# Optimization experiments

Measured on AMD Instinct MI355X. Metric: run time of the kernel, lower is better.

The kernel has to match this reference:

```python
import jax, jax.numpy as jnp
import numpy as np

B, S, H, DH = 1, 4096, 8, 40  # hardcoded in the original forward
D = H * DH  # 320

def setup_inputs() -> dict:
    key = jax.random.key(0)
    ks = jax.random.split(key, 6)
    s = 1.0 / np.sqrt(D)
    return {
        "x": jax.random.normal(ks[0], (B, S, D), dtype=jnp.float32),
        "Wq": jax.random.normal(ks[1], (D, D), dtype=jnp.float32) * s,
        "Wk": jax.random.normal(ks[2], (D, D), dtype=jnp.float32) * s,
        "Wv": jax.random.normal(ks[3], (D, D), dtype=jnp.float32) * s,
        "Wo": jax.random.normal(ks[4], (D, D), dtype=jnp.float32) * s,
        "bo": jnp.zeros((D,), dtype=jnp.float32),
    }

def reference(x, Wq, Wk, Wv, Wo, bo):
    scale = DH ** (-0.5)
    # nn.Linear(bias=False): y = x @ W^T. context = x (self-attention).
    q = x @ Wq.T
    k = x @ Wk.T
    v = x @ Wv.T
    # split heads: [B,S,D] -> [B*H, S, DH]
    def split_heads(t):
        return t.reshape(B, S, H, DH).transpose(0, 2, 1, 3).reshape(B * H, S, DH)
    q, k, v = split_heads(q), split_heads(k), split_heads(v)
    # fp32 QK^T (original forces float), softmax, AV
    sim = jnp.einsum('bid,bjd->bij', q.astype(jnp.float32), k.astype(jnp.float32)) * scale
    attn = jax.nn.softmax(sim, axis=-1)
    out = jnp.einsum('bij,bjd->bid', attn, v)
    # merge heads: [B*H, S, DH] -> [B, S, D]
    out = out.reshape(B, H, S, DH).transpose(0, 2, 1, 3).reshape(B, S, D)
    return out @ Wo.T + bo
```

## Files before the change

kernel.cpp:

```cpp
#include <hip/hip_runtime.h>
#include <math.h>


#define NS 4096
#define ND 320
#define SCALE2 0.2281101152f
#define HS48 196608
#define VTH 163840
#define XN 1310720

typedef __attribute__((ext_vector_type(8))) short bf16x8;
typedef __attribute__((ext_vector_type(16))) float f32x16;

static __device__ __forceinline__ unsigned short f2bru(float f) {
  return (unsigned short)((__builtin_bit_cast(unsigned int, f) + 0x8000u) >> 16);
}
static __device__ __forceinline__ unsigned int pk2ru(float a, float b) {
  unsigned int ua = __builtin_bit_cast(unsigned int, a) + 0x8000u;
  unsigned int ub = __builtin_bit_cast(unsigned int, b) + 0x8000u;
  return __builtin_amdgcn_perm(ub, ua, 0x07060302u);
}
static __device__ __forceinline__ unsigned int pk2t(float a, float b) {
  return __builtin_amdgcn_perm(__builtin_bit_cast(unsigned int, b),
                               __builtin_bit_cast(unsigned int, a), 0x07060302u);
}
static __device__ __forceinline__ float fexp2(float x) {
  return __builtin_amdgcn_exp2f(x);
}
static __device__ __forceinline__ bf16x8 ld8(const unsigned short* p) {
  union { uint2 u[2]; bf16x8 v; } c;
  c.u[0] = *(const uint2*)p;
  c.u[1] = *(const uint2*)(p + 4);
  return c.v;
}
static __device__ __forceinline__ uint4 ld16u(const unsigned short* p) {
  uint2 a = *(const uint2*)p, b = *(const uint2*)(p + 4);
  return make_uint4(a.x, a.y, b.x, b.y);
}
static __device__ __forceinline__ void st16(unsigned short* p, uint4 v) {
  *(uint2*)p = make_uint2(v.x, v.y);
  *(uint2*)(p + 4) = make_uint2(v.z, v.w);
}
static __device__ __forceinline__ int sig32(int q) {
  int s = q >> 4, h2 = (q >> 3) & 1, j = q & 7;
  return (s << 4) | ((j >> 2) << 3) | (h2 << 2) | (j & 3);
}

__global__ __launch_bounds__(256) void proj_qkv_kernel(
    const float* __restrict__ x, const float* __restrict__ Wq,
    const float* __restrict__ Wk, const float* __restrict__ Wv,
    unsigned short* __restrict__ Qp, unsigned short* __restrict__ Kp,
    unsigned short* __restrict__ Vt) {
  const int zi = blockIdx.y;
  const int z = zi / 5;
  const int bnn = (zi - z * 5) * 64;
  const float* W = (z == 0) ? Wq : (z == 1) ? Wk : Wv;
  __shared__ __align__(16) unsigned short As[128 * 76];
  __shared__ __align__(16) unsigned short Bs[64 * 76];
  const int t = threadIdx.x;
  const int w = t >> 6, l = t & 63, l31 = l & 31, hi = l >> 5;
  const int bm = blockIdx.x * 128;
  const int m0 = w * 32;
  f32x16 acc0 = {0,0,0,0,0,0,0,0,0,0,0,0,0,0,0,0};
  f32x16 acc1 = {0,0,0,0,0,0,0,0,0,0,0,0,0,0,0,0};
  const unsigned short* af = As + (m0 + l31) * 76 + hi * 8;
  const unsigned short* bf0 = Bs + l31 * 76 + hi * 8;
  const unsigned short* bf1 = Bs + (32 + l31) * 76 + hi * 8;
  for (int k0 = 0; k0 < ND; k0 += 64) {
    __syncthreads();
#pragma unroll
    for (int i = 0; i < 4; i++) {
      int c = t + i * 256;
      int row = c >> 3, kc = (c & 7) << 3;
      const float* g = x + (bm + row) * ND + k0 + kc;
      float4 v0 = *(const float4*)g, v1 = *(const float4*)(g + 4);
      st16(As + row * 76 + kc,
           make_uint4(pk2ru(v0.x, v0.y), pk2ru(v0.z, v0.w),
                      pk2ru(v1.x, v1.y), pk2ru(v1.z, v1.w)));
    }
#pragma unroll
    for (int i = 0; i < 2; i++) {
      int c = t + i * 256;
      int row = c >> 3, kc = (c & 7) << 3;
      const float* g = W + (bnn + row) * ND + k0 + kc;
      float4 v0 = *(const float4*)g, v1 = *(const float4*)(g + 4);
      st16(Bs + row * 76 + kc,
           make_uint4(pk2ru(v0.x, v0.y), pk2ru(v0.z, v0.w),
                      pk2ru(v1.x, v1.y), pk2ru(v1.z, v1.w)));
    }
    __syncthreads();
#pragma unroll
    for (int ks = 0; ks < 4; ks++) {
      bf16x8 A = ld8(af + ks * 16);
      acc0 = __builtin_amdgcn_mfma_f32_32x32x16_bf16(A, ld8(bf0 + ks * 16), acc0, 0, 0, 0);
      acc1 = __builtin_amdgcn_mfma_f32_32x32x16_bf16(A, ld8(bf1 + ks * 16), acc1, 0, 0, 0);
    }
  }
  __syncthreads();
  if (z < 2) {
    unsigned short* Tile = As;
    unsigned short* Y = (z == 0) ? Qp : Kp;
    const float sc = (z == 0) ? SCALE2 : 1.0f;
    const unsigned int padw = (z == 0) ? 0xC200u : 0x3F80u;
#pragma unroll
    for (int r2 = 0; r2 < 16; r2++) {
      int lr = m0 + (r2 & 3) + 8 * (r2 >> 2) + 4 * hi;
      Tile[lr * 68 + l31] = f2bru(acc0[r2] * sc);
      Tile[lr * 68 + 32 + l31] = f2bru(acc1[r2] * sc);
    }
    __syncthreads();
#pragma unroll
    for (int i = 0; i < 4; i++) {
      int c = t + i * 256;
      int row = c >> 3, ch = c & 7;
      int j = bnn + ch * 8;
      int h = j / 40, dh = j - h * 40;
      uint4 v = ld16u(Tile + row * 68 + ch * 8);
      st16(Y + h * HS48 + (bm + row) * 48 + dh, v);
      if (dh == 0)
        st16(Y + h * HS48 + (bm + row) * 48 + 40, make_uint4(padw, 0u, 0u, 0u));
    }
  } else {
    unsigned short* Tile = As;
#pragma unroll
    for (int r2 = 0; r2 < 16; r2++) {
      int lr = m0 + (r2 & 3) + 8 * (r2 >> 2) + 4 * hi;
      Tile[l31 * 132 + lr] = f2bru(acc0[r2]);
      Tile[(32 + l31) * 132 + lr] = f2bru(acc1[r2]);
    }
    __syncthreads();
#pragma unroll
    for (int i = 0; i < 4; i++) {
      int c = t + i * 256;
      int row = c >> 4, ch = c & 15;
      int j = bnn + row;
      int h = j / 40, dd = j - h * 40;
      uint4 v = ld16u(Tile + row * 132 + ch * 8);
      st16(Vt + h * VTH + dd * NS + bm + ch * 8, v);
    }
  }
}

__global__ __launch_bounds__(256) void attn_kernel(
    const unsigned short* __restrict__ Qp, const unsigned short* __restrict__ Kp,
    const unsigned short* __restrict__ Vt, unsigned short* __restrict__ Op,
    float* __restrict__ Lp) {
  const int b = blockIdx.x;
  const int h = b & 7, ks = (b >> 3) & 7, qt = b >> 6;
  const int t = threadIdx.x;
  const int w = t >> 6, l = t & 63, l31 = l & 31, hi = l >> 5;
  __shared__ __align__(16) unsigned short Ks[64 * 68];
  __shared__ __align__(16) unsigned short Vs[48 * 68];
  for (int i = t; i < 272; i += 256)
    ((unsigned int*)(Vs + 40 * 68))[i] = (i < 34) ? 0x3F803F80u : 0u;

  const int kbase = ks * 512;
  const int qbase = qt * 128 + w * 32;
  const unsigned short* qp = Qp + h * HS48 + (qbase + l31) * 48 + hi * 8;
  bf16x8 qf0 = *(const bf16x8*)qp;
  bf16x8 qf1 = *(const bf16x8*)(qp + 16);
  bf16x8 qf2 = *(const bf16x8*)(qp + 32);

  f32x16 oa0 = {0,0,0,0,0,0,0,0,0,0,0,0,0,0,0,0};
  f32x16 oa1 = {0,0,0,0,0,0,0,0,0,0,0,0,0,0,0,0};

  const int kr0 = t / 6, kc0 = t - kr0 * 6;
  const int kr1 = (t + 256) / 6, kc1 = (t + 256) - kr1 * 6;
  const unsigned short* gK0 = Kp + h * HS48 + (kbase + kr0) * 48 + kc0 * 8;
  const unsigned short* gK1 = Kp + h * HS48 + (kbase + kr1) * 48 + kc1 * 8;
  unsigned short* lK0 = Ks + ((kr0 & 32) | sig32(kr0 & 31)) * 68 + kc0 * 8;
  unsigned short* lK1 = Ks + ((kr1 & 32) | sig32(kr1 & 31)) * 68 + kc1 * 8;
  const int vr0 = t >> 3, vc = t & 7, vr1 = 32 + vr0;
  const unsigned short* gV0 = Vt + h * VTH + vr0 * NS + kbase + vc * 8;
  const unsigned short* gV1 = Vt + h * VTH + vr1 * NS + kbase + vc * 8;
  unsigned short* lV0 = Vs + vr0 * 68 + vc * 8;
  unsigned short* lV1 = Vs + vr1 * 68 + vc * 8;

  const unsigned short* kf0 = Ks + l31 * 68 + hi * 8;
  const unsigned short* kf1 = Ks + (32 + l31) * 68 + hi * 8;
  const unsigned short* vf0 = Vs + l31 * 68 + hi * 8;
  const unsigned short* vf1 = Vs + (32 + (l31 & 15)) * 68 + hi * 8;

  uint4 ka = *(const uint4*)gK0;
  uint4 kb2, vb2;
  uint4 va = *(const uint4*)gV0;
  if (t < 128) kb2 = *(const uint4*)gK1;
  if (t < 64)  vb2 = *(const uint4*)gV1;

  for (int it = 0; it < 8; ++it) {
    __syncthreads();
    st16(lK0, ka);
    if (t < 128) st16(lK1, kb2);
    st16(lV0, va);
    if (t < 64) st16(lV1, vb2);
    __syncthreads();
    gK0 += 64 * 48; gK1 += 64 * 48; gV0 += 64; gV1 += 64;
    ka = *(const uint4*)gK0;
    va = *(const uint4*)gV0;
    if (t < 128) kb2 = *(const uint4*)gK1;
    if (t < 64)  vb2 = *(const uint4*)gV1;

    {
      f32x16 s0 = {0,0,0,0,0,0,0,0,0,0,0,0,0,0,0,0};
      s0 = __builtin_amdgcn_mfma_f32_32x32x16_bf16(ld8(kf0), qf0, s0, 0, 0, 0);
      s0 = __builtin_amdgcn_mfma_f32_32x32x16_bf16(ld8(kf0 + 16), qf1, s0, 0, 0, 0);
      s0 = __builtin_amdgcn_mfma_f32_32x32x16_bf16(ld8(kf0 + 32), qf2, s0, 0, 0, 0);
      unsigned int pw[8];
#pragma unroll
      for (int i = 0; i < 8; i++)
        pw[i] = pk2t(fexp2(s0[2 * i]), fexp2(s0[2 * i + 1]));
      bf16x8 pf0 = __builtin_bit_cast(bf16x8, make_uint4(pw[0], pw[1], pw[2], pw[3]));
      bf16x8 pf1 = __builtin_bit_cast(bf16x8, make_uint4(pw[4], pw[5], pw[6], pw[7]));
      oa0 = __builtin_amdgcn_mfma_f32_32x32x16_bf16(pf0, ld8(vf0), oa0, 0, 0, 0);
      oa1 = __builtin_amdgcn_mfma_f32_32x32x16_bf16(pf0, ld8(vf1), oa1, 0, 0, 0);
      oa0 = __builtin_amdgcn_mfma_f32_32x32x16_bf16(pf1, ld8(vf0 + 16), oa0, 0, 0, 0);
      oa1 = __builtin_amdgcn_mfma_f32_32x32x16_bf16(pf1, ld8(vf1 + 16), oa1, 0, 0, 0);
    }
    {
      f32x16 s1 = {0,0,0,0,0,0,0,0,0,0,0,0,0,0,0,0};
      s1 = __builtin_amdgcn_mfma_f32_32x32x16_bf16(ld8(kf1), qf0, s1, 0, 0, 0);
      s1 = __builtin_amdgcn_mfma_f32_32x32x16_bf16(ld8(kf1 + 16), qf1, s1, 0, 0, 0);
      s1 = __builtin_amdgcn_mfma_f32_32x32x16_bf16(ld8(kf1 + 32), qf2, s1, 0, 0, 0);
      unsigned int pw[8];
#pragma unroll
      for (int i = 0; i < 8; i++)
        pw[i] = pk2t(fexp2(s1[2 * i]), fexp2(s1[2 * i + 1]));
      bf16x8 pf2 = __builtin_bit_cast(bf16x8, make_uint4(pw[0], pw[1], pw[2], pw[3]));
      bf16x8 pf3 = __builtin_bit_cast(bf16x8, make_uint4(pw[4], pw[5], pw[6], pw[7]));
      oa0 = __builtin_amdgcn_mfma_f32_32x32x16_bf16(pf2, ld8(vf0 + 32), oa0, 0, 0, 0);
      oa1 = __builtin_amdgcn_mfma_f32_32x32x16_bf16(pf2, ld8(vf1 + 32), oa1, 0, 0, 0);
      oa0 = __builtin_amdgcn_mfma_f32_32x32x16_bf16(pf3, ld8(vf0 + 48), oa0, 0, 0, 0);
      oa1 = __builtin_amdgcn_mfma_f32_32x32x16_bf16(pf3, ld8(vf1 + 48), oa1, 0, 0, 0);
    }
  }

  unsigned short* opb = Op + ks * XN + h * 163840;
  float* lpb = Lp + ks * 32768 + h * NS;
#pragma unroll
  for (int r2 = 0; r2 < 16; r2++) {
    int qr = qbase + (r2 & 3) + 8 * (r2 >> 2) + 4 * hi;
    opb[qr * 40 + l31] = f2bru(oa0[r2]);
    if (l31 < 8) opb[qr * 40 + 32 + l31] = f2bru(oa1[r2]);
    if (l31 == 8) lpb[qr] = oa1[r2];
  }
}

__global__ __launch_bounds__(256) void combine_kernel(
    const unsigned short* __restrict__ Op, const float* __restrict__ Lp,
    unsigned short* __restrict__ Xo) {
  int e = (blockIdx.x * 256 + threadIdx.x) * 2;
  int h = e / 163840;
  int r = e - h * 163840;
  int s = r / 40;
  int dh = r - s * 40;
  float a0 = 0.f, a1 = 0.f, lsum = 0.f;
#pragma unroll
  for (int k = 0; k < 8; k++) {
    unsigned int u = *(const unsigned int*)(Op + k * XN + e);
    a0 += __builtin_bit_cast(float, u << 16);
    a1 += __builtin_bit_cast(float, u & 0xFFFF0000u);
    lsum += Lp[k * 32768 + h * NS + s];
  }
  float inv = 1.0f / lsum;
  *(unsigned int*)(Xo + s * ND + h * 40 + dh) = pk2ru(a0 * inv, a1 * inv);
}

__global__ __launch_bounds__(256) void proj_out_kernel(
    const unsigned short* __restrict__ Xo, const float* __restrict__ Wo,
    const float* __restrict__ bo, float* __restrict__ out) {
  __shared__ __align__(16) unsigned short As[128 * 76];
  __shared__ __align__(16) unsigned short Bs[64 * 76];
  const int t = threadIdx.x;
  const int w = t >> 6, l = t & 63, l31 = l & 31, hi = l >> 5;
  const int bm = blockIdx.x * 128;
  const int bnn = blockIdx.y * 64;
  const int m0 = w * 32;
  f32x16 acc0 = {0,0,0,0,0,0,0,0,0,0,0,0,0,0,0,0};
  f32x16 acc1 = {0,0,0,0,0,0,0,0,0,0,0,0,0,0,0,0};
  const unsigned short* af = As + (m0 + l31) * 76 + hi * 8;
  const unsigned short* bf0 = Bs + l31 * 76 + hi * 8;
  const unsigned short* bf1 = Bs + (32 + l31) * 76 + hi * 8;
  for (int k0 = 0; k0 < ND; k0 += 64) {
    __syncthreads();
#pragma unroll
    for (int i = 0; i < 4; i++) {
      int c = t + i * 256;
      int row = c >> 3, kc = (c & 7) << 3;
      uint4 v = *(const uint4*)(Xo + (bm + row) * ND + k0 + kc);
      st16(As + row * 76 + kc, v);
    }
#pragma unroll
    for (int i = 0; i < 2; i++) {
      int c = t + i * 256;
      int row = c >> 3, kc = (c & 7) << 3;
      const float* g = Wo + (bnn + row) * ND + k0 + kc;
      float4 v0 = *(const float4*)g, v1 = *(const float4*)(g + 4);
      st16(Bs + row * 76 + kc,
           make_uint4(pk2ru(v0.x, v0.y), pk2ru(v0.z, v0.w),
                      pk2ru(v1.x, v1.y), pk2ru(v1.z, v1.w)));
    }
    __syncthreads();
#pragma unroll
    for (int ks = 0; ks < 4; ks++) {
      bf16x8 A = ld8(af + ks * 16);
      acc0 = __builtin_amdgcn_mfma_f32_32x32x16_bf16(A, ld8(bf0 + ks * 16), acc0, 0, 0, 0);
      acc1 = __builtin_amdgcn_mfma_f32_32x32x16_bf16(A, ld8(bf1 + ks * 16), acc1, 0, 0, 0);
    }
  }
  const int j0 = bnn + l31, j1 = bnn + 32 + l31;
  const float bj0 = bo[j0], bj1 = bo[j1];
#pragma unroll
  for (int r2 = 0; r2 < 16; r2++) {
    int row = bm + m0 + (r2 & 3) + 8 * (r2 >> 2) + 4 * hi;
    out[row * ND + j0] = acc0[r2] + bj0;
    out[row * ND + j1] = acc1[r2] + bj1;
  }
}

extern "C" void kernel_launch(void* const* d_in, const int* in_sizes, int n_in,
                              void* d_out, int out_size, void* d_ws, size_t ws_size,
                              hipStream_t stream) {
  (void)in_sizes; (void)n_in; (void)out_size; (void)ws_size;
  const float* x  = (const float*)d_in[0];
  const float* Wq = (const float*)d_in[1];
  const float* Wk = (const float*)d_in[2];
  const float* Wv = (const float*)d_in[3];
  const float* Wo = (const float*)d_in[4];
  const float* bo = (const float*)d_in[5];
  float* out = (float*)d_out;

  unsigned short* Qp = (unsigned short*)d_ws;
  unsigned short* Kp = Qp + 8 * HS48;
  unsigned short* Vt = Kp + 8 * HS48;
  unsigned short* Xo = Vt + 8 * VTH;
  unsigned short* Op = Xo + XN;
  float* Lp = (float*)(Op + 8 * XN);

  proj_qkv_kernel<<<dim3(32, 15), 256, 0, stream>>>(x, Wq, Wk, Wv, Qp, Kp, Vt);
  attn_kernel<<<dim3(2048), 256, 0, stream>>>(Qp, Kp, Vt, Op, Lp);
  combine_kernel<<<dim3(2560), 256, 0, stream>>>(Op, Lp, Xo);
  proj_out_kernel<<<dim3(32, 5), 256, 0, stream>>>(Xo, Wo, bo, out);
}
```

Measured before the change: 131.3 us.

## Double-buffer K/V tiles in LDS and halve attention key splits

The attention kernel now uses a single LDS buffer split into two halves. The next K/V tile is written to one half while the current half feeds the MFMAs, which cuts the two barriers per iteration down to one. The key dimension is split into 4 chunks of 1024 instead of 8 of 512, halving the number of blocks and the partial outputs the combine kernel has to sum. Fewer blocks means less parallelism and longer per-block loops, and the larger LDS footprint may limit occupancy.

```diff
diff --git a/kernel.cpp b/kernel.cpp
--- a/kernel.cpp
+++ b/kernel.cpp
@@ -141,68 +141,88 @@
   }
 }
 
-__global__ __launch_bounds__(256) void attn_kernel(
+__global__ __launch_bounds__(256, 4) void attn_kernel(
     const unsigned short* __restrict__ Qp, const unsigned short* __restrict__ Kp,
     const unsigned short* __restrict__ Vt, unsigned short* __restrict__ Op,
     float* __restrict__ Lp) {
   const int b = blockIdx.x;
-  const int h = b & 7, ks = (b >> 3) & 7, qt = b >> 6;
+  const int h = b & 7, ks = (b >> 3) & 3, qt = b >> 5;
   const int t = threadIdx.x;
   const int w = t >> 6, l = t & 63, l31 = l & 31, hi = l >> 5;
-  __shared__ __align__(16) unsigned short Ks[64 * 68];
-  __shared__ __align__(16) unsigned short Vs[48 * 68];
-  for (int i = t; i < 272; i += 256)
-    ((unsigned int*)(Vs + 40 * 68))[i] = (i < 34) ? 0x3F803F80u : 0u;
-
-  const int kbase = ks * 512;
+  __shared__ __align__(16) unsigned short Lds[16384];
+  for (int i = t; i < 544; i += 256) {
+    int bsel = (i >= 272) ? 1 : 0;
+    int ui = i - bsel * 272;
+    ((unsigned int*)(Lds + bsel * 8192 + 4352 + 40 * 68))[ui] =
+        (ui < 34) ? 0x3F803F80u : 0u;
+  }
+
+  const int kbase = ks * 1024;
   const int qbase = qt * 128 + w * 32;
   const unsigned short* qp = Qp + h * HS48 + (qbase + l31) * 48 + hi * 8;
   bf16x8 qf0 = *(const bf16x8*)qp;
   bf16x8 qf1 = *(const bf16x8*)(qp + 16);
   bf16x8 qf2 = *(const bf16x8*)(qp + 32);
 
-  f32x16 oa0 = {0,0,0,0,0,0,0,0,0,0,0,0,0,0,0,0};
-  f32x16 oa1 = {0,0,0,0,0,0,0,0,0,0,0,0,0,0,0,0};
-
+  const f32x16 Z = {0,0,0,0,0,0,0,0,0,0,0,0,0,0,0,0};
+  f32x16 oa0 = Z, oa1 = Z;
+
+  const int id1 = t + 256;
+  const bool has2 = (t < 192);
   const int kr0 = t / 6, kc0 = t - kr0 * 6;
-  const int kr1 = (t + 256) / 6, kc1 = (t + 256) - kr1 * 6;
-  const unsigned short* gK0 = Kp + h * HS48 + (kbase + kr0) * 48 + kc0 * 8;
-  const unsigned short* gK1 = Kp + h * HS48 + (kbase + kr1) * 48 + kc1 * 8;
-  unsigned short* lK0 = Ks + ((kr0 & 32) | sig32(kr0 & 31)) * 68 + kc0 * 8;
-  unsigned short* lK1 = Ks + ((kr1 & 32) | sig32(kr1 & 31)) * 68 + kc1 * 8;
-  const int vr0 = t >> 3, vc = t & 7, vr1 = 32 + vr0;
-  const unsigned short* gV0 = Vt + h * VTH + vr0 * NS + kbase + vc * 8;
-  const unsigned short* gV1 = Vt + h * VTH + vr1 * NS + kbase + vc * 8;
-  unsigned short* lV0 = Vs + vr0 * 68 + vc * 8;
-  unsigned short* lV1 = Vs + vr1 * 68 + vc * 8;
-
-  const unsigned short* kf0 = Ks + l31 * 68 + hi * 8;
-  const unsigned short* kf1 = Ks + (32 + l31) * 68 + hi * 8;
-  const unsigned short* vf0 = Vs + l31 * 68 + hi * 8;
-  const unsigned short* vf1 = Vs + (32 + (l31 & 15)) * 68 + hi * 8;
-
-  uint4 ka = *(const uint4*)gK0;
-  uint4 kb2, vb2;
-  uint4 va = *(const uint4*)gV0;
-  if (t < 128) kb2 = *(const uint4*)gK1;
-  if (t < 64)  vb2 = *(const uint4*)gV1;
-
-  for (int it = 0; it < 8; ++it) {
-    __syncthreads();
-    st16(lK0, ka);
-    if (t < 128) st16(lK1, kb2);
-    st16(lV0, va);
-    if (t < 64) st16(lV1, vb2);
-    __syncthreads();
-    gK0 += 64 * 48; gK1 += 64 * 48; gV0 += 64; gV1 += 64;
-    ka = *(const uint4*)gK0;
-    va = *(const uint4*)gV0;
-    if (t < 128) kb2 = *(const uint4*)gK1;
-    if (t < 64)  vb2 = *(const uint4*)gV1;
+  const unsigned short* g0 = Kp + h * HS48 + (kbase + kr0) * 48 + kc0 * 8;
+  const int w0 = ((kr0 & 32) | sig32(kr0 & 31)) * 68 + kc0 * 8;
+  const unsigned short* g1;
+  int w1, inc1;
+  if (id1 < 384) {
+    int kr = id1 / 6, kc = id1 - kr * 6;
+    g1 = Kp + h * HS48 + (kbase + kr) * 48 + kc * 8;
+    w1 = ((kr & 32) | sig32(kr & 31)) * 68 + kc * 8;
+    inc1 = 64 * 48;
+  } else {
+    int vid = id1 - 384, vr = vid >> 3, vc = vid & 7;
+    g1 = Vt + h * VTH + vr * NS + kbase + vc * 8;
+    w1 = 4352 + vr * 68 + vc * 8;
+    inc1 = 64;
+  }
+  const int vid2 = t + 128;
+  const int vr2 = vid2 >> 3, vc2 = vid2 & 7;
+  const unsigned short* g2 = Vt + h * VTH + vr2 * NS + kbase + vc2 * 8;
+  const int w2 = 4352 + vr2 * 68 + vc2 * 8;
+
+  const int rk  = l31 * 68 + hi * 8;
+  const int rv0 = 4352 + l31 * 68 + hi * 8;
+  const int rv1 = 4352 + (32 + (l31 & 15)) * 68 + hi * 8;
+
+  uint4 r0 = *(const uint4*)g0; g0 += 3072;
+  uint4 r1 = *(const uint4*)g1; g1 += inc1;
+  uint4 r2{};
+  if (has2) { r2 = *(const uint4*)g2; g2 += 64; }
+  st16(Lds + w0, r0);
+  st16(Lds + w1, r1);
+  if (has2) st16(Lds + w2, r2);
+  r0 = *(const uint4*)g0; g0 += 3072;
+  r1 = *(const uint4*)g1; g1 += inc1;
+  if (has2) { r2 = *(const uint4*)g2; g2 += 64; }
+  __syncthreads();
+
+  for (int it = 0; it < 16; ++it) {
+    const int bo = (it & 1) << 13;
+    const int bn = bo ^ 8192;
+    st16(Lds + bn + w0, r0);
+    st16(Lds + bn + w1, r1);
+    if (has2) st16(Lds + bn + w2, r2);
+    r0 = *(const uint4*)g0; g0 += 3072;
+    r1 = *(const uint4*)g1; g1 += inc1;
+    if (has2) { r2 = *(const uint4*)g2; g2 += 64; }
+
+    const unsigned short* kf0 = Lds + bo + rk;
+    const unsigned short* kf1 = kf0 + 2176;
+    const unsigned short* vf0 = Lds + bo + rv0;
+    const unsigned short* vf1 = Lds + bo + rv1;
 
     {
-      f32x16 s0 = {0,0,0,0,0,0,0,0,0,0,0,0,0,0,0,0};
-      s0 = __builtin_amdgcn_mfma_f32_32x32x16_bf16(ld8(kf0), qf0, s0, 0, 0, 0);
+      f32x16 s0 = __builtin_amdgcn_mfma_f32_32x32x16_bf16(ld8(kf0), qf0, Z, 0, 0, 0);
       s0 = __builtin_amdgcn_mfma_f32_32x32x16_bf16(ld8(kf0 + 16), qf1, s0, 0, 0, 0);
       s0 = __builtin_amdgcn_mfma_f32_32x32x16_bf16(ld8(kf0 + 32), qf2, s0, 0, 0, 0);
       unsigned int pw[8];
@@ -217,8 +237,7 @@
       oa1 = __builtin_amdgcn_mfma_f32_32x32x16_bf16(pf1, ld8(vf1 + 16), oa1, 0, 0, 0);
     }
     {
-      f32x16 s1 = {0,0,0,0,0,0,0,0,0,0,0,0,0,0,0,0};
-      s1 = __builtin_amdgcn_mfma_f32_32x32x16_bf16(ld8(kf1), qf0, s1, 0, 0, 0);
+      f32x16 s1 = __builtin_amdgcn_mfma_f32_32x32x16_bf16(ld8(kf1), qf0, Z, 0, 0, 0);
       s1 = __builtin_amdgcn_mfma_f32_32x32x16_bf16(ld8(kf1 + 16), qf1, s1, 0, 0, 0);
       s1 = __builtin_amdgcn_mfma_f32_32x32x16_bf16(ld8(kf1 + 32), qf2, s1, 0, 0, 0);
       unsigned int pw[8];
@@ -232,16 +251,17 @@
       oa0 = __builtin_amdgcn_mfma_f32_32x32x16_bf16(pf3, ld8(vf0 + 48), oa0, 0, 0, 0);
       oa1 = __builtin_amdgcn_mfma_f32_32x32x16_bf16(pf3, ld8(vf1 + 48), oa1, 0, 0, 0);
     }
+    __syncthreads();
   }
 
   unsigned short* opb = Op + ks * XN + h * 163840;
   float* lpb = Lp + ks * 32768 + h * NS;
 #pragma unroll
-  for (int r2 = 0; r2 < 16; r2++) {
-    int qr = qbase + (r2 & 3) + 8 * (r2 >> 2) + 4 * hi;
-    opb[qr * 40 + l31] = f2bru(oa0[r2]);
-    if (l31 < 8) opb[qr * 40 + 32 + l31] = f2bru(oa1[r2]);
-    if (l31 == 8) lpb[qr] = oa1[r2];
+  for (int r2i = 0; r2i < 16; r2i++) {
+    int qr = qbase + (r2i & 3) + 8 * (r2i >> 2) + 4 * hi;
+    opb[qr * 40 + l31] = f2bru(oa0[r2i]);
+    if (l31 < 8) opb[qr * 40 + 32 + l31] = f2bru(oa1[r2i]);
+    if (l31 == 8) lpb[qr] = oa1[r2i];
   }
 }
 
@@ -255,7 +275,7 @@
   int dh = r - s * 40;
   float a0 = 0.f, a1 = 0.f, lsum = 0.f;
 #pragma unroll
-  for (int k = 0; k < 8; k++) {
+  for (int k = 0; k < 4; k++) {
     unsigned int u = *(const unsigned int*)(Op + k * XN + e);
     a0 += __builtin_bit_cast(float, u << 16);
     a1 += __builtin_bit_cast(float, u & 0xFFFF0000u);
@@ -334,10 +354,10 @@
   unsigned short* Vt = Kp + 8 * HS48;
   unsigned short* Xo = Vt + 8 * VTH;
   unsigned short* Op = Xo + XN;
-  float* Lp = (float*)(Op + 8 * XN);
+  float* Lp = (float*)(Op + 4 * XN);
 
   proj_qkv_kernel<<<dim3(32, 15), 256, 0, stream>>>(x, Wq, Wk, Wv, Qp, Kp, Vt);
-  attn_kernel<<<dim3(2048), 256, 0, stream>>>(Qp, Kp, Vt, Op, Lp);
+  attn_kernel<<<dim3(1024), 256, 0, stream>>>(Qp, Kp, Vt, Op, Lp);
   combine_kernel<<<dim3(2560), 256, 0, stream>>>(Op, Lp, Xo);
   proj_out_kernel<<<dim3(32, 5), 256, 0, stream>>>(Xo, Wo, bo, out);
 }
```

Measured after the change: 120.7 us. -8.1%, faster.
